# Performance work log

Measured on AMD Instinct MI355X. Metric: run time of the kernel, lower is better.

Reference implementation:

```python
import jax, jax.numpy as jnp
import numpy as np

B, C, H, T, K = 8, 512, 512, 4096, 2


def _conv1d_causal(x, w, b):
    # x: [B, C, T], w: [H, C, K] (torch Conv1d layout OIH), causal left-pad K-1 zeros
    k = w.shape[-1]
    y = jax.lax.conv_general_dilated(
        x, w, window_strides=(1,), padding=[(k - 1, 0)],
        dimension_numbers=("NCH", "OIH", "NCH"))
    return y + b[None, :, None]


def setup_inputs() -> dict:
    key = jax.random.key(0)
    ks = jax.random.split(key, 5)
    scale = 1.0 / np.sqrt(C * K)  # torch Conv1d default init scale
    inp = {"x": jax.random.normal(ks[0], (B, C, T), dtype=jnp.float32)}
    for name, k in zip("zfoi", ks[1:]):
        inp["w" + name] = jax.random.uniform(k, (H, C, K), jnp.float32, -scale, scale)
        inp["b" + name] = jnp.zeros((H,), jnp.float32)
    return inp


def reference(x, wz, bz, wf, bf, wo, bo, wi, bi):
    # QRNN 'ifo' pooling: c_t = f_t * c_{t-1} + i_t * z_t;  h_t = o_t * c_t
    z = jnp.tanh(_conv1d_causal(x, wz, bz))
    f = jax.nn.sigmoid(_conv1d_causal(x, wf, bf))  # zoneout p=0 -> identity
    o = jax.nn.sigmoid(_conv1d_causal(x, wo, bo))
    i = jax.nn.sigmoid(_conv1d_causal(x, wi, bi))
    g = i * z  # [B, H, T]

    fT = jnp.moveaxis(f, 2, 0)  # [T, B, H]
    gT = jnp.moveaxis(g, 2, 0)

    def step(c, fg):
        ft, gt = fg
        c = ft * c + gt
        return c, c

    c0 = jnp.zeros((x.shape[0], wz.shape[0]), dtype=x.dtype)
    _, cT = jax.lax.scan(step, c0, (fT, gT))
    c = jnp.moveaxis(cT, 0, 2)  # [B, H, T]
    return o * c
```

## Files before the change

kernel.cpp:

```cpp
#include <hip/hip_runtime.h>
#include <hip/hip_bf16.h>
#include <cstdint>

typedef _Float16 half8 __attribute__((ext_vector_type(8)));
typedef float f32x4 __attribute__((ext_vector_type(4)));

#define B_DIM 8
#define C_DIM 512
#define H_DIM 512
#define T_DIM 4096
#define KTOT 1024
#define MTOT 2048

__device__ __forceinline__ void gload16(const void* g, void* l) {
  __builtin_amdgcn_global_load_lds(
      (const __attribute__((address_space(1))) unsigned int*)g,
      (__attribute__((address_space(3))) unsigned int*)l, 16, 0, 0);
}

__device__ __forceinline__ float sigmoidf_(float x) { return 1.0f / (1.0f + expf(-x)); }

__global__ __launch_bounds__(256) void prep(
    const float* __restrict__ x,
    const float* __restrict__ wz, const float* __restrict__ wf,
    const float* __restrict__ wo, const float* __restrict__ wi,
    _Float16* __restrict__ XTg, _Float16* __restrict__ A16) {
  __shared__ _Float16 tile[64][73];
  int bid = blockIdx.x;
  int tid = threadIdx.x;
  if (bid < 4096) {
    int b = bid >> 9;
    int rem = bid & 511;
    int c0 = (rem >> 6) * 64;
    int t0 = (rem & 63) * 64;
#pragma unroll
    for (int it = 0; it < 4; ++it) {
      int idx = it * 256 + tid;
      int ci = idx >> 4, tc = idx & 15;
      float4 v = *(const float4*)(x + (((size_t)b * C_DIM + c0 + ci) * T_DIM + t0 + tc * 4));
      tile[ci][tc * 4 + 0] = (_Float16)v.x;
      tile[ci][tc * 4 + 1] = (_Float16)v.y;
      tile[ci][tc * 4 + 2] = (_Float16)v.z;
      tile[ci][tc * 4 + 3] = (_Float16)v.w;
    }
    __syncthreads();
#pragma unroll
    for (int it = 0; it < 2; ++it) {
      int idx = it * 256 + tid;
      int tr = idx >> 3, cb = idx & 7;
      half8 h;
#pragma unroll
      for (int e = 0; e < 8; ++e) h[e] = tile[cb * 8 + e][tr];
      int t = t0 + tr;
      *(half8*)(XTg + ((size_t)b * (T_DIM + 1) + 1 + t) * 512 + c0 + cb * 8) = h;
    }
    if (t0 == 0 && tid < 8) {
      half8 z = {};
      *(half8*)(XTg + ((size_t)b * (T_DIM + 1)) * 512 + c0 + tid * 8) = z;
    }
  } else {
    int idx = (bid - 4096) * 256 + tid;
    int m = idx >> 9, c = idx & 511;
    int h = m >> 2, g = m & 3;
    const float* w = (g == 0) ? wz : (g == 1) ? wf : (g == 2) ? wo : wi;
    float2 v = *(const float2*)(w + (h << 10) + (c << 1));
    A16[(size_t)m * KTOT + c] = (_Float16)v.x;
    A16[(size_t)m * KTOT + 512 + c] = (_Float16)v.y;
  }
}

__global__ __launch_bounds__(256, 4) void qrnn_gemm(
    const _Float16* __restrict__ A16, const _Float16* __restrict__ XTg,
    const float* __restrict__ bz, const float* __restrict__ bf,
    const float* __restrict__ bo, const float* __restrict__ bi,
    _Float16* __restrict__ F, _Float16* __restrict__ G, _Float16* __restrict__ O) {
  __shared__ _Float16 lA[128 * 64];
  __shared__ _Float16 lB[128 * 64];
  int bid = blockIdx.x;
  int gbid = (bid & 7) * 512 + (bid >> 3);
  int b = gbid >> 9;
  int rem = gbid & 511;
  int m0 = (rem >> 5) * 128;
  int t0 = (rem & 31) * 128;
  int tid = threadIdx.x;
  int lane = tid & 63, wid = tid >> 6;
  int wm = (wid >> 1) * 64, wn = (wid & 1) * 64;

  f32x4 acc[4][4];
#pragma unroll
  for (int i = 0; i < 4; ++i)
#pragma unroll
    for (int j = 0; j < 4; ++j) acc[i][j] = (f32x4){0.f, 0.f, 0.f, 0.f};

  const _Float16* Ab = A16 + (size_t)m0 * KTOT;
  const _Float16* Bb = XTg + ((size_t)b * (T_DIM + 1) + 1 + t0) * 512;

  for (int kt = 0; kt < 16; ++kt) {
    int k0 = kt * 64;
    int cp = k0 & 511;
    int jofs = (k0 < 512) ? 512 : 0;
#pragma unroll
    for (int it = 0; it < 4; ++it) {
      int idx = it * 256 + tid;
      int row = idx >> 3, blk = idx & 7;
      int gblk = blk ^ (row & 7);
      gload16(Ab + (size_t)row * KTOT + k0 + gblk * 8, (char*)lA + idx * 16);
    }
#pragma unroll
    for (int it = 0; it < 4; ++it) {
      int idx = it * 256 + tid;
      int row = idx >> 3, blk = idx & 7;
      int gblk = blk ^ (row & 7);
      gload16(Bb + (size_t)(row * 512) - jofs + cp + gblk * 8, (char*)lB + idx * 16);
    }
    __syncthreads();
#pragma unroll
    for (int ks = 0; ks < 2; ++ks) {
      half8 av[4], bv[4];
#pragma unroll
      for (int i = 0; i < 4; ++i) {
        int row = wm + i * 16 + (lane & 15);
        int blk = (ks * 4 + (lane >> 4)) ^ (row & 7);
        av[i] = *(const half8*)(lA + row * 64 + blk * 8);
      }
#pragma unroll
      for (int j = 0; j < 4; ++j) {
        int row = wn + j * 16 + (lane & 15);
        int blk = (ks * 4 + (lane >> 4)) ^ (row & 7);
        bv[j] = *(const half8*)(lB + row * 64 + blk * 8);
      }
#pragma unroll
      for (int i = 0; i < 4; ++i)
#pragma unroll
        for (int j = 0; j < 4; ++j)
          acc[i][j] = __builtin_amdgcn_mfma_f32_16x16x32_f16(av[i], bv[j], acc[i][j], 0, 0, 0);
    }
    __syncthreads();
  }

#pragma unroll
  for (int i = 0; i < 4; ++i) {
    int h = ((m0 + wm + i * 16) >> 2) + (lane >> 4);
    float vbz = bz[h], vbf = bf[h], vbo = bo[h], vbi = bi[h];
#pragma unroll
    for (int j = 0; j < 4; ++j) {
      int t = t0 + wn + j * 16 + (lane & 15);
      float yz = acc[i][j][0] + vbz;
      float yf = acc[i][j][1] + vbf;
      float yo = acc[i][j][2] + vbo;
      float yi = acc[i][j][3] + vbi;
      float zz = tanhf(yz);
      float ff = sigmoidf_(yf);
      float oo = sigmoidf_(yo);
      float ii = sigmoidf_(yi);
      size_t gi = ((size_t)b * H_DIM + h) * T_DIM + t;
      F[gi] = (_Float16)ff;
      G[gi] = (_Float16)(ii * zz);
      O[gi] = (_Float16)oo;
    }
  }
}

__global__ __launch_bounds__(256) void scan_fused(
    const _Float16* __restrict__ F, const _Float16* __restrict__ G,
    const _Float16* __restrict__ O, float* __restrict__ out) {
  __shared__ char smem[24 * 1024 + 64];
  _Float16* sF = (_Float16*)smem;
  _Float16* sG = (_Float16*)(smem + 8192);
  _Float16* sO = (_Float16*)(smem + 16384);
  float* sOut = (float*)smem;
  float* wFs = (float*)(smem + 24576);
  float* wGs = wFs + 4;

  int tid = threadIdx.x;
  int lane = tid & 63, wv = tid >> 6;
  size_t base = (size_t)blockIdx.x * T_DIM;
  const _Float16* Fg = F + base;
  const _Float16* Gg = G + base;
  const _Float16* Og = O + base;

#pragma unroll
  for (int it = 0; it < 2; ++it) {
    int idx = it * 256 + tid;
    int sb = idx ^ ((idx >> 3) & 7);
    gload16(Fg + sb * 8, (char*)sF + idx * 16);
    gload16(Gg + sb * 8, (char*)sG + idx * 16);
    gload16(Og + sb * 8, (char*)sO + idx * 16);
  }
  asm volatile("s_waitcnt vmcnt(0)" ::: "memory");
  __syncthreads();

  int i = tid;
  int b0 = (2 * i) ^ (((2 * i) >> 3) & 7);
  int b1 = (2 * i + 1) ^ (((2 * i + 1) >> 3) & 7);
  half8 f0 = *(half8*)((char*)sF + b0 * 16);
  half8 f1 = *(half8*)((char*)sF + b1 * 16);
  half8 g0 = *(half8*)((char*)sG + b0 * 16);
  half8 g1 = *(half8*)((char*)sG + b1 * 16);
  half8 o0 = *(half8*)((char*)sO + b0 * 16);
  half8 o1 = *(half8*)((char*)sO + b1 * 16);

  float Fp = 1.f, Gc = 0.f;
#pragma unroll
  for (int e = 0; e < 8; ++e) {
    float fe = (float)f0[e];
    Gc = fe * Gc + (float)g0[e];
    Fp *= fe;
  }
#pragma unroll
  for (int e = 0; e < 8; ++e) {
    float fe = (float)f1[e];
    Gc = fe * Gc + (float)g1[e];
    Fp *= fe;
  }

  float Fs = Fp, Gs = Gc;
#pragma unroll
  for (int d = 1; d < 64; d <<= 1) {
    float Fo = __shfl_up(Fs, d);
    float Go = __shfl_up(Gs, d);
    if (lane >= d) { Gs = Fs * Go + Gs; Fs = Fs * Fo; }
  }
  if (lane == 63) { wFs[wv] = Fs; wGs[wv] = Gs; }
  __syncthreads();
  float carry = 0.f;
  for (int w = 0; w < wv; ++w) carry = wFs[w] * carry + wGs[w];
  float Fpr = __shfl_up(Fs, 1);
  float Gpr = __shfl_up(Gs, 1);
  float cin = (lane == 0) ? carry : Fpr * carry + Gpr;

  float c = cin;
  float4 r0, r1, r2, r3;
#define QSTEP(fv, gv, ov, e, dst) \
  { c = (float)fv[e] * c + (float)gv[e]; dst = (float)ov[e] * c; }
  QSTEP(f0, g0, o0, 0, r0.x) QSTEP(f0, g0, o0, 1, r0.y)
  QSTEP(f0, g0, o0, 2, r0.z) QSTEP(f0, g0, o0, 3, r0.w)
  QSTEP(f0, g0, o0, 4, r1.x) QSTEP(f0, g0, o0, 5, r1.y)
  QSTEP(f0, g0, o0, 6, r1.z) QSTEP(f0, g0, o0, 7, r1.w)
  QSTEP(f1, g1, o1, 0, r2.x) QSTEP(f1, g1, o1, 1, r2.y)
  QSTEP(f1, g1, o1, 2, r2.z) QSTEP(f1, g1, o1, 3, r2.w)
  QSTEP(f1, g1, o1, 4, r3.x) QSTEP(f1, g1, o1, 5, r3.y)
  QSTEP(f1, g1, o1, 6, r3.z) QSTEP(f1, g1, o1, 7, r3.w)
#undef QSTEP
  {
    int obl = 4 * i;
    int s0 = (obl + 0) ^ (((obl + 0) >> 3) & 7);
    int s1 = (obl + 1) ^ (((obl + 1) >> 3) & 7);
    int s2 = (obl + 2) ^ (((obl + 2) >> 3) & 7);
    int s3 = (obl + 3) ^ (((obl + 3) >> 3) & 7);
    *(float4*)((char*)sOut + s0 * 16) = r0;
    *(float4*)((char*)sOut + s1 * 16) = r1;
    *(float4*)((char*)sOut + s2 * 16) = r2;
    *(float4*)((char*)sOut + s3 * 16) = r3;
  }
  __syncthreads();

  float* og = out + base;
#pragma unroll
  for (int it = 0; it < 4; ++it) {
    int idx = it * 256 + tid;
    int sb = idx ^ ((idx >> 3) & 7);
    *(float4*)(og + idx * 4) = *(float4*)((char*)sOut + sb * 16);
  }
}

extern "C" void kernel_launch(void* const* d_in, const int* in_sizes, int n_in,
                              void* d_out, int out_size, void* d_ws, size_t ws_size,
                              hipStream_t stream) {
  (void)in_sizes; (void)n_in; (void)out_size; (void)ws_size;
  const float* x  = (const float*)d_in[0];
  const float* wz = (const float*)d_in[1];
  const float* bz = (const float*)d_in[2];
  const float* wf = (const float*)d_in[3];
  const float* bf = (const float*)d_in[4];
  const float* wo = (const float*)d_in[5];
  const float* bo = (const float*)d_in[6];
  const float* wi = (const float*)d_in[7];
  const float* bi = (const float*)d_in[8];

  char* ws = (char*)d_ws;
  const size_t MB = 1ull << 20;
  _Float16* A16 = (_Float16*)(ws);
  _Float16* XTg = (_Float16*)(ws + 4 * MB);
  _Float16* F   = (_Float16*)(ws + 40 * MB);
  _Float16* G   = (_Float16*)(ws + 72 * MB);
  _Float16* O   = (_Float16*)(ws + 104 * MB);

  prep<<<4096 + 4096, 256, 0, stream>>>(x, wz, wf, wo, wi, XTg, A16);
  qrnn_gemm<<<B_DIM * 16 * 32, 256, 0, stream>>>(A16, XTg, bz, bf, bo, bi, F, G, O);
  scan_fused<<<B_DIM * H_DIM, 256, 0, stream>>>(F, G, O, (float*)d_out);
}
```

Before: 327.1 us.

## Interleave F/G/O rows into one buffer, drop XCD block remap, relax launch bounds

Stores the three gate tensors interleaved per (batch, hidden) row in a single buffer, so each scan block loads one contiguous 24KB region with a single loop instead of three separate streams. The GEMM drops its XCD-aware block index remap and lowers the launch-bounds occupancy hint from 4 to 2 blocks per CU, which gives the compiler more registers. The intent is better DRAM locality in the scan and fewer spills in the GEMM. The risk is lost L2 locality across XCDs and lower occupancy for the GEMM.

```diff
diff --git a/kernel.cpp b/kernel.cpp
--- a/kernel.cpp
+++ b/kernel.cpp
@@ -69,17 +69,16 @@
   }
 }
 
-__global__ __launch_bounds__(256, 4) void qrnn_gemm(
+__global__ __launch_bounds__(256, 2) void qrnn_gemm(
     const _Float16* __restrict__ A16, const _Float16* __restrict__ XTg,
     const float* __restrict__ bz, const float* __restrict__ bf,
     const float* __restrict__ bo, const float* __restrict__ bi,
-    _Float16* __restrict__ F, _Float16* __restrict__ G, _Float16* __restrict__ O) {
+    _Float16* __restrict__ FGO) {
   __shared__ _Float16 lA[128 * 64];
   __shared__ _Float16 lB[128 * 64];
   int bid = blockIdx.x;
-  int gbid = (bid & 7) * 512 + (bid >> 3);
-  int b = gbid >> 9;
-  int rem = gbid & 511;
+  int b = bid >> 9;
+  int rem = bid & 511;
   int m0 = (rem >> 5) * 128;
   int t0 = (rem & 31) * 128;
   int tid = threadIdx.x;
@@ -142,6 +141,7 @@
   for (int i = 0; i < 4; ++i) {
     int h = ((m0 + wm + i * 16) >> 2) + (lane >> 4);
     float vbz = bz[h], vbf = bf[h], vbo = bo[h], vbi = bi[h];
+    size_t rowbase = ((size_t)b * H_DIM + h) * (3 * T_DIM);
 #pragma unroll
     for (int j = 0; j < 4; ++j) {
       int t = t0 + wn + j * 16 + (lane & 15);
@@ -153,17 +153,15 @@
       float ff = sigmoidf_(yf);
       float oo = sigmoidf_(yo);
       float ii = sigmoidf_(yi);
-      size_t gi = ((size_t)b * H_DIM + h) * T_DIM + t;
-      F[gi] = (_Float16)ff;
-      G[gi] = (_Float16)(ii * zz);
-      O[gi] = (_Float16)oo;
+      FGO[rowbase + t] = (_Float16)ff;
+      FGO[rowbase + T_DIM + t] = (_Float16)(ii * zz);
+      FGO[rowbase + 2 * T_DIM + t] = (_Float16)oo;
     }
   }
 }
 
 __global__ __launch_bounds__(256) void scan_fused(
-    const _Float16* __restrict__ F, const _Float16* __restrict__ G,
-    const _Float16* __restrict__ O, float* __restrict__ out) {
+    const _Float16* __restrict__ FGO, float* __restrict__ out) {
   __shared__ char smem[24 * 1024 + 64];
   _Float16* sF = (_Float16*)smem;
   _Float16* sG = (_Float16*)(smem + 8192);
@@ -174,18 +172,13 @@
 
   int tid = threadIdx.x;
   int lane = tid & 63, wv = tid >> 6;
-  size_t base = (size_t)blockIdx.x * T_DIM;
-  const _Float16* Fg = F + base;
-  const _Float16* Gg = G + base;
-  const _Float16* Og = O + base;
-
-#pragma unroll
-  for (int it = 0; it < 2; ++it) {
+  const _Float16* src = FGO + (size_t)blockIdx.x * (3 * T_DIM);
+
+#pragma unroll
+  for (int it = 0; it < 6; ++it) {
     int idx = it * 256 + tid;
     int sb = idx ^ ((idx >> 3) & 7);
-    gload16(Fg + sb * 8, (char*)sF + idx * 16);
-    gload16(Gg + sb * 8, (char*)sG + idx * 16);
-    gload16(Og + sb * 8, (char*)sO + idx * 16);
+    gload16(src + sb * 8, smem + idx * 16);
   }
   asm volatile("s_waitcnt vmcnt(0)" ::: "memory");
   __syncthreads();
@@ -255,7 +248,7 @@
   }
   __syncthreads();
 
-  float* og = out + base;
+  float* og = out + (size_t)blockIdx.x * T_DIM;
 #pragma unroll
   for (int it = 0; it < 4; ++it) {
     int idx = it * 256 + tid;
@@ -282,11 +275,9 @@
   const size_t MB = 1ull << 20;
   _Float16* A16 = (_Float16*)(ws);
   _Float16* XTg = (_Float16*)(ws + 4 * MB);
-  _Float16* F   = (_Float16*)(ws + 40 * MB);
-  _Float16* G   = (_Float16*)(ws + 72 * MB);
-  _Float16* O   = (_Float16*)(ws + 104 * MB);
+  _Float16* FGO = (_Float16*)(ws + 40 * MB);
 
   prep<<<4096 + 4096, 256, 0, stream>>>(x, wz, wf, wo, wi, XTg, A16);
-  qrnn_gemm<<<B_DIM * 16 * 32, 256, 0, stream>>>(A16, XTg, bz, bf, bo, bi, F, G, O);
-  scan_fused<<<B_DIM * H_DIM, 256, 0, stream>>>(F, G, O, (float*)d_out);
-}
+  qrnn_gemm<<<B_DIM * 16 * 32, 256, 0, stream>>>(A16, XTg, bz, bf, bo, bi, FGO);
+  scan_fused<<<B_DIM * H_DIM, 256, 0, stream>>>(FGO, (float*)d_out);
+}
```

Measured after the change: 317.9 us. 2.8% less time.
